# Performance work log

Measured on AMD Instinct MI355X. Metric: run time of the kernel, lower is better.

## Reference

```python
import jax, jax.numpy as jnp
import numpy as np

B, CIN, H, W = 32, 512, 16, 16
COUT, HEADS, SPARSITY = 2048, 8, 7
D = COUT // HEADS  # 256, must equal H*W
N = H * W


def conv1x1(x, w, b):
    # x: [B,C,H,W], w: [O,C], b: [O]
    return jnp.einsum('bchw,oc->bohw', x, w) + b[None, :, None, None]


def setup_inputs() -> dict:
    key = jax.random.key(0)
    ks = jax.random.split(key, 11)
    def lin(k, o, c):
        bound = 1.0 / np.sqrt(c)
        kw, kb = jax.random.split(k)
        return (jax.random.uniform(kw, (o, c), jnp.float32, -bound, bound),
                jax.random.uniform(kb, (o,), jnp.float32, -bound, bound))
    Wq, bq = lin(ks[0], COUT, CIN)
    Wk, bk = lin(ks[1], COUT, CIN)
    Wv, bv = lin(ks[2], COUT, CIN)
    Wo, bo = lin(ks[3], COUT, COUT)
    # kaiming_uniform_ on [COUT, COUT]
    gain = np.sqrt(2.0) / np.sqrt(5.0)  # default a=sqrt(5)
    bound = gain * np.sqrt(3.0 / COUT)
    coeff = jax.random.uniform(ks[4], (COUT, COUT), jnp.float32, -bound, bound)
    scale = jnp.array([np.sqrt(D)], jnp.float32)
    x = jax.random.normal(ks[5], (B, CIN, H, W), jnp.float32)
    return {"x": x, "Wq": Wq, "bq": bq, "Wk": Wk, "bk": bk, "Wv": Wv,
            "bv": bv, "Wo": Wo, "bo": bo, "coeff": coeff, "scale": scale}


def reference(x, Wq, bq, Wk, bk, Wv, bv, Wo, bo, coeff, scale):
    # enforce_sparsity: keep top-`SPARSITY` |coeff| per row, zero the rest
    _, idx = jax.lax.top_k(jnp.abs(coeff), SPARSITY)  # [COUT, SPARSITY]
    mask = jnp.zeros(coeff.shape, bool).at[jnp.arange(COUT)[:, None], idx].set(True)
    coeff_s = jnp.where(mask, coeff, 0.0)

    q = conv1x1(x, Wq, bq).reshape(B, HEADS, D, N)
    k = conv1x1(x, Wk, bk).reshape(B, HEADS, D, N)
    v = conv1x1(x, Wv, bv).reshape(B, HEADS, D, N)

    attn = jnp.einsum('bhdn,bhdm->bhnm', q, k) / scale[0]  # [B,h,N,N]
    sparse_attn = jnp.einsum('bhnm,mp->bhnp', attn, coeff_s[:D, :D])
    sparse_attn = jax.nn.softmax(sparse_attn, axis=-1)
    out = jnp.einsum('bhnm,bhmd->bhnd', sparse_attn, v.transpose(0, 1, 3, 2))
    out = out.transpose(0, 1, 3, 2).reshape(B, COUT, H, W)
    return conv1x1(out, Wo, bo)
```

## Files before the change

kernel.cpp:

```cpp
#include <hip/hip_runtime.h>

typedef unsigned short ushort;
typedef __attribute__((ext_vector_type(8))) short short8;
typedef __attribute__((ext_vector_type(8))) unsigned short ushort8;
typedef __attribute__((ext_vector_type(4))) unsigned short ushort4v;
typedef __attribute__((ext_vector_type(4))) float fx4;

#define MAXNNZ (256*7)

__device__ __forceinline__ ushort f2bf(float f) {
    union { float f; unsigned u; } v; v.f = f;
    unsigned r = v.u + 0x7fffu + ((v.u >> 16) & 1u);
    return (ushort)(r >> 16);
}

__device__ __forceinline__ float bf2f(ushort b) {
    union { unsigned u; float f; } v; v.u = ((unsigned)b) << 16;
    return v.f;
}

__device__ __forceinline__ void gload_lds16(const ushort* g, ushort* l) {
    __builtin_amdgcn_global_load_lds(
        (const __attribute__((address_space(1))) unsigned int*)g,
        (__attribute__((address_space(3))) unsigned int*)l, 16, 0, 0);
}

__global__ __launch_bounds__(256)
void topk_kernel(const float* __restrict__ coeff,
                 int* __restrict__ coo_cnt, int* __restrict__ coo_m,
                 int* __restrict__ coo_p, float* __restrict__ coo_v)
{
    int row = blockIdx.x;
    int tid = threadIdx.x;
    const float* crow = coeff + (long)row * 2048;
    float av[8];
#pragma unroll
    for (int i = 0; i < 8; ++i) av[i] = fabsf(crow[tid + 256 * i]);
    __shared__ unsigned long long red[256];
    for (int t = 0; t < 7; ++t) {
        float mx = -1.f; int mi = 0;
#pragma unroll
        for (int i = 0; i < 8; ++i) if (av[i] > mx) { mx = av[i]; mi = i; }
        unsigned col = (unsigned)(tid + 256 * mi);
        unsigned long long pk = ((unsigned long long)__float_as_uint(mx) << 32)
                              | (unsigned long long)(2048u - col);
        red[tid] = pk; __syncthreads();
        for (int s = 128; s > 0; s >>= 1) {
            if (tid < s) { if (red[tid + s] > red[tid]) red[tid] = red[tid + s]; }
            __syncthreads();
        }
        unsigned long long w = red[0];
        __syncthreads();
        unsigned wcol = 2048u - (unsigned)(w & 0xffffffffu);
        if ((wcol & 255u) == (unsigned)tid) av[wcol >> 8] = -1.f;
        if (tid == 0 && wcol < 256u) {
            int pos = atomicAdd(coo_cnt, 1);
            coo_m[pos] = row; coo_p[pos] = (int)wcol; coo_v[pos] = crow[wcol];
        }
    }
}

__global__ __launch_bounds__(256)
void csc_kernel(const int* __restrict__ coo_cnt, const int* __restrict__ coo_m,
                const int* __restrict__ coo_p, const float* __restrict__ coo_v,
                int* __restrict__ csc_ptr, int* __restrict__ csc_m, float* __restrict__ csc_v)
{
    __shared__ int cnt[256];
    __shared__ int off[257];
    __shared__ int cur[256];
    int tid = threadIdx.x;
    cnt[tid] = 0;
    __syncthreads();
    int n = *coo_cnt; if (n > MAXNNZ) n = MAXNNZ;
    for (int e = tid; e < n; e += 256) atomicAdd(&cnt[coo_p[e]], 1);
    __syncthreads();
    if (tid == 0) {
        int s = 0;
        for (int p = 0; p < 256; ++p) { off[p] = s; s += cnt[p]; }
        off[256] = s;
    }
    __syncthreads();
    csc_ptr[tid] = off[tid];
    if (tid == 0) csc_ptr[256] = off[256];
    cur[tid] = off[tid];
    __syncthreads();
    for (int e = tid; e < n; e += 256) {
        int p = coo_p[e];
        int pos = atomicAdd(&cur[p], 1);
        csc_m[pos] = coo_m[e];
        csc_v[pos] = coo_v[e];
    }
}

__global__ void cvt4_kernel(const float* a0, ushort* d0, int n0,
                            const float* a1, ushort* d1, int n1,
                            const float* a2, ushort* d2, int n2,
                            const float* a3, ushort* d3, int n3)
{
    const float* s; ushort* d; int n;
    switch (blockIdx.y) {
        case 0: s = a0; d = d0; n = n0; break;
        case 1: s = a1; d = d1; n = n1; break;
        case 2: s = a2; d = d2; n = n2; break;
        default: s = a3; d = d3; n = n3; break;
    }
    int nv = n >> 2;
    for (int i = blockIdx.x * blockDim.x + threadIdx.x; i < nv; i += gridDim.x * blockDim.x) {
        fx4 v = ((const fx4*)s)[i];
        ushort4v o;
        o[0] = f2bf(v[0]); o[1] = f2bf(v[1]); o[2] = f2bf(v[2]); o[3] = f2bf(v[3]);
        ((ushort4v*)d)[i] = o;
    }
}

__global__ __launch_bounds__(256)
void transpose_f32_bf16(const float* __restrict__ in, ushort* __restrict__ out, int R, int C)
{
    int z = blockIdx.z;
    const float* ib = in + (long)z * R * C;
    ushort* ob = out + (long)z * R * C;
    __shared__ ushort tile[64][72];
    int r0 = blockIdx.x * 64, c0 = blockIdx.y * 64;
    int tid = threadIdx.x;
    int rl = tid >> 2, sg = tid & 3;
#pragma unroll
    for (int h = 0; h < 4; ++h) {
        fx4 v = *(const fx4*)(ib + (long)(r0 + rl) * C + c0 + h * 16 + sg * 4);
#pragma unroll
        for (int i = 0; i < 4; ++i) tile[h * 16 + sg * 4 + i][rl] = f2bf(v[i]);
    }
    __syncthreads();
    int cl = rl;
#pragma unroll
    for (int h = 0; h < 2; ++h) {
        ushort8 vv = *(const ushort8*)(&tile[cl][h * 32 + sg * 8]);
        *(ushort8*)(ob + (long)(c0 + cl) * R + r0 + h * 32 + sg * 8) = vv;
    }
}

__global__ __launch_bounds__(256)
void kcomb_kernel(const ushort* __restrict__ kbT, ushort* __restrict__ ktc,
                  const int* __restrict__ csc_ptr, const int* __restrict__ csc_m,
                  const float* __restrict__ csc_v)
{
    int z = blockIdx.y;
    int tid = threadIdx.x;
    int p = blockIdx.x * 64 + (tid >> 2);
    int d0 = (tid & 3) * 64;
    const ushort* src = kbT + (long)z * 65536;
    float acc[64];
#pragma unroll
    for (int i = 0; i < 64; ++i) acc[i] = 0.f;
    int e0 = csc_ptr[p], e1 = csc_ptr[p + 1];
    for (int e = e0; e < e1; ++e) {
        const ushort* row = src + csc_m[e] * 256 + d0;
        float c = csc_v[e];
#pragma unroll
        for (int u = 0; u < 8; ++u) {
            ushort8 v = *(const ushort8*)(row + u * 8);
#pragma unroll
            for (int t = 0; t < 8; ++t) acc[u * 8 + t] += bf2f(v[t]) * c;
        }
    }
    ushort* dst = ktc + (long)z * 65536 + (long)p * 256 + d0;
#pragma unroll
    for (int u = 0; u < 8; ++u) {
        ushort8 o;
#pragma unroll
        for (int t = 0; t < 8; ++t) o[t] = f2bf(acc[u * 8 + t]);
        *(ushort8*)(dst + u * 8) = o;
    }
}

template<int MODE>
__global__ __launch_bounds__(256)
void gemm128(const ushort* __restrict__ A, long long strideA,
             const ushort* __restrict__ B, long long strideB,
             void* __restrict__ C,
             const float* __restrict__ bias0, const float* __restrict__ bias1,
             const float* __restrict__ bias2,
             int N, int K)
{
    int z = blockIdx.z;
    const ushort* Ab = A + (long long)z * strideA;
    const ushort* Bb = B + (long long)z * strideB;
    int m0 = blockIdx.x * 128, n0 = blockIdx.y * 128;

    __shared__ __align__(16) ushort As[128 * 32];
    __shared__ __align__(16) ushort Bs[128 * 32];
    __shared__ __align__(16) ushort Ct[(MODE == 3) ? 128 * 136 : 8];

    int tid = threadIdx.x;
    int wave = tid >> 6, lane = tid & 63;
    int wrow = wave >> 1, wcol = wave & 1;
    int l16 = lane & 15, quad = lane >> 4;
    int lrow = lane >> 2, lkq = lane & 3;

    fx4 acc[4][4];
#pragma unroll
    for (int i = 0; i < 4; ++i)
#pragma unroll
        for (int j = 0; j < 4; ++j) acc[i][j] = (fx4){0.f, 0.f, 0.f, 0.f};

    const ushort* gA0 = Ab + (long)(m0 + wave * 16 + lrow) * K + lkq * 8;
    const ushort* gA1 = gA0 + (long)64 * K;
    const ushort* gB0 = Bb + (long)(n0 + wave * 16 + lrow) * K + lkq * 8;
    const ushort* gB1 = gB0 + (long)64 * K;
    ushort* lA0 = As + (wave * 16) * 32;
    ushort* lA1 = As + (64 + wave * 16) * 32;
    ushort* lB0 = Bs + (wave * 16) * 32;
    ushort* lB1 = Bs + (64 + wave * 16) * 32;

    for (int kc = 0; kc < K; kc += 32) {
        __syncthreads();
        gload_lds16(gA0 + kc, lA0);
        gload_lds16(gA1 + kc, lA1);
        gload_lds16(gB0 + kc, lB0);
        gload_lds16(gB1 + kc, lB1);
        __syncthreads();

        short8 af[4], bf[4];
#pragma unroll
        for (int i = 0; i < 4; ++i)
            af[i] = *(const short8*)(As + (wrow * 64 + i * 16 + l16) * 32 + quad * 8);
#pragma unroll
        for (int j = 0; j < 4; ++j)
            bf[j] = *(const short8*)(Bs + (wcol * 64 + j * 16 + l16) * 32 + quad * 8);
#pragma unroll
        for (int i = 0; i < 4; ++i)
#pragma unroll
            for (int j = 0; j < 4; ++j)
                acc[i][j] = __builtin_amdgcn_mfma_f32_16x16x32_bf16(af[i], bf[j], acc[i][j], 0, 0, 0);
    }

    if (MODE == 3) {
#pragma unroll
        for (int i = 0; i < 4; ++i)
#pragma unroll
            for (int j = 0; j < 4; ++j) {
                int ml = wrow * 64 + i * 16 + quad * 4;
                int nl = wcol * 64 + j * 16 + l16;
                ushort4v pk;
#pragma unroll
                for (int r = 0; r < 4; ++r) pk[r] = f2bf(acc[i][j][r]);
                *(ushort4v*)(Ct + nl * 136 + ml) = pk;
            }
        __syncthreads();
        long long zb = z >> 3; int zh = z & 7;
        int nl = tid >> 3, mc = (tid & 7) * 16;
#pragma unroll
        for (int p4 = 0; p4 < 4; ++p4) {
            int n = p4 * 32 + nl;
            ushort8 v0 = *(const ushort8*)(Ct + n * 136 + mc);
            ushort8 v1 = *(const ushort8*)(Ct + n * 136 + mc + 8);
            ushort* dst = (ushort*)C + zb * 524288 + (long)(n0 + n) * 2048
                        + zh * 256 + m0 + mc;
            *(ushort8*)dst = v0;
            *(ushort8*)(dst + 8) = v1;
        }
        return;
    }
}

template<int MODE>
__global__ __launch_bounds__(512, 2)
void gemm256(const ushort* __restrict__ A, const ushort* __restrict__ B,
             void* __restrict__ C,
             const float* __restrict__ bias0, const float* __restrict__ bias1,
             const float* __restrict__ bias2,
             int MT, int K)
{
    __shared__ __align__(16) ushort lds[4][2][8192];

    int nwg = gridDim.x;
    int bid = blockIdx.x;
    int cpx = nwg >> 3;
    int swz = (bid & 7) * cpx + (bid >> 3);
    int mt = swz % MT, nt = swz / MT;
    int m0 = mt << 8, n0 = nt << 8;

    int tid = threadIdx.x;
    int wave = tid >> 6, lane = tid & 63;
    int wr = wave >> 2, wc = wave & 3;
    int l16 = lane & 15, quad = lane >> 4;

    int lc = (((lane & 3) ^ ((lane >> 3) & 3))) * 8;
    const ushort* gA0 = A + (long long)(m0 + wave * 16 + (lane >> 2)) * K + lc;
    const ushort* gA1 = gA0 + (long long)128 * K;
    const ushort* gB0 = B + (long long)(n0 + wave * 16 + (lane >> 2)) * K + lc;
    const ushort* gB1 = gB0 + (long long)128 * K;
    int ldso = wave * 512;

    int rsw = ((l16 >> 1) & 3) * 8;
    int aoff = (wr * 128 + l16) * 32 + ((quad * 8) ^ rsw);
    int boff = (wc * 64 + l16) * 32 + ((quad * 8) ^ rsw);

    fx4 acc[8][4];
#pragma unroll
    for (int i = 0; i < 8; ++i)
#pragma unroll
        for (int j = 0; j < 4; ++j) acc[i][j] = (fx4){0.f, 0.f, 0.f, 0.f};

    auto stageA = [&](int b, int kc) {
        gload_lds16(gA0 + kc, &lds[b][0][ldso]);
        gload_lds16(gA1 + kc, &lds[b][0][4096 + ldso]);
    };
    auto stageB = [&](int b, int kc) {
        gload_lds16(gB0 + kc, &lds[b][1][ldso]);
        gload_lds16(gB1 + kc, &lds[b][1][4096 + ldso]);
    };

    short8 af[4], bf[4];
    auto readA = [&](int b, int half) {
        const ushort* p = &lds[b][0][aoff + half * 2048];
#pragma unroll
        for (int i = 0; i < 4; ++i) af[i] = *(const short8*)(p + i * 512);
    };
    auto readB = [&](int b) {
        const ushort* p = &lds[b][1][boff];
#pragma unroll
        for (int j = 0; j < 4; ++j) bf[j] = *(const short8*)(p + j * 512);
    };
    auto mma = [&](int half) {
        __builtin_amdgcn_s_setprio(1);
#pragma unroll
        for (int i = 0; i < 4; ++i)
#pragma unroll
            for (int j = 0; j < 4; ++j)
                acc[half * 4 + i][j] =
                    __builtin_amdgcn_mfma_f32_16x16x32_bf16(af[i], bf[j], acc[half * 4 + i][j], 0, 0, 0);
        __builtin_amdgcn_s_setprio(0);
    };

    int NT = K >> 5;
    stageA(0, 0);  stageB(0, 0);
    stageA(1, 32); stageB(1, 32);
    stageA(2, 64); stageB(2, 64);
    asm volatile("s_waitcnt vmcnt(8)" ::: "memory");
    __builtin_amdgcn_s_barrier();

    for (int t = 0; t < NT; ++t) {
        int b = t & 3;
        readA(b, 0); readB(b);
        if (t + 3 < NT) stageA((t + 3) & 3, (t + 3) << 5);
        __builtin_amdgcn_s_barrier();
        asm volatile("s_waitcnt lgkmcnt(0)" ::: "memory");
        __builtin_amdgcn_sched_barrier(0);
        mma(0);
        __builtin_amdgcn_s_barrier();
        readA(b, 1);
        if (t + 3 < NT) {
            stageB((t + 3) & 3, (t + 3) << 5);
            asm volatile("s_waitcnt vmcnt(8)" ::: "memory");
        } else if (t + 2 < NT) {
            asm volatile("s_waitcnt vmcnt(4)" ::: "memory");
        } else if (t + 1 < NT) {
            asm volatile("s_waitcnt vmcnt(0)" ::: "memory");
        }
        __builtin_amdgcn_s_barrier();
        asm volatile("s_waitcnt lgkmcnt(0)" ::: "memory");
        __builtin_amdgcn_sched_barrier(0);
        mma(1);
        __builtin_amdgcn_s_barrier();
    }

    if (MODE == 5) {
        float* Cf = (float*)C + (long long)nt * 524288;
#pragma unroll
        for (int i = 0; i < 8; ++i) {
            int m = m0 + wr * 128 + i * 16 + quad * 4;
#pragma unroll
            for (int j = 0; j < 4; ++j) {
                int n = wc * 64 + j * 16 + l16;
                float* dst = Cf + (long long)m * 256 + n;
#pragma unroll
                for (int r = 0; r < 4; ++r)
                    dst[(long)r * 256] = acc[i][j][r] + bias0[m + r];
            }
        }
        return;
    }

    if (MODE == 4) {
        int sec = m0 >> 11;
        int ms0 = m0 & 2047;
        ushort* ct = &lds[0][0][0];
        if (sec < 2) {
            const float* bs = (sec == 0) ? bias0 : bias1;
            ushort* base = (ushort*)C + (long long)sec * 16777216
                         + (long long)nt * 524288 + (long long)(ms0 >> 8) * 65536;
#pragma unroll
            for (int hh = 0; hh < 2; ++hh) {
                if ((wc >> 1) == hh) {
#pragma unroll
                    for (int i = 0; i < 8; ++i)
#pragma unroll
                        for (int j = 0; j < 4; ++j) {
                            int nl = (wc & 1) * 64 + j * 16 + l16;
                            int ml = wr * 128 + i * 16 + quad * 4;
                            ushort4v pk;
#pragma unroll
                            for (int r = 0; r < 4; ++r)
                                pk[r] = f2bf(acc[i][j][r] + bs[ms0 + ml + r]);
                            *(ushort4v*)(ct + nl * 264 + ml) = pk;
                        }
                }
                __syncthreads();
                int row = tid & 127, c0 = (tid >> 7) * 64;
                ushort* dst = base + (long long)(hh * 128 + row) * 256 + c0;
                const ushort* src = ct + row * 264 + c0;
#pragma unroll
                for (int u = 0; u < 8; ++u)
                    *(ushort8*)(dst + u * 8) = *(const ushort8*)(src + u * 8);
                __syncthreads();
            }
        } else {
            ushort* base = (ushort*)C + 33554432LL + (long long)nt * 524288
                         + (long long)ms0 * 256;
#pragma unroll
            for (int hh = 0; hh < 2; ++hh) {
                if (wr == hh) {
#pragma unroll
                    for (int i = 0; i < 8; ++i)
#pragma unroll
                        for (int j = 0; j < 4; ++j) {
                            int nl = wc * 64 + j * 16 + l16;
                            int ml = i * 16 + quad * 4;
#pragma unroll
                            for (int r = 0; r < 4; ++r)
                                ct[(ml + r) * 264 + nl] =
                                    f2bf(acc[i][j][r] + bias2[ms0 + hh * 128 + ml + r]);
                        }
                }
                __syncthreads();
                int row = tid & 127, c0 = (tid >> 7) * 64;
                ushort* dst = base + (long long)(hh * 128 + row) * 256 + c0;
                const ushort* src = ct + row * 264 + c0;
#pragma unroll
                for (int u = 0; u < 8; ++u)
                    *(ushort8*)(dst + u * 8) = *(const ushort8*)(src + u * 8);
                __syncthreads();
            }
        }
        return;
    }
}

__global__ __launch_bounds__(256)
void tsm_kernel(const ushort* __restrict__ Q, const ushort* __restrict__ Kt,
                ushort* __restrict__ P, const float* __restrict__ scale_src)
{
    int z = blockIdx.y;
    const ushort* Ab = Q + (long)z * 65536;
    const ushort* Bb = Kt + (long)z * 65536;
    int n0 = blockIdx.x * 128;

    __shared__ __align__(16) ushort As[128 * 32];
    __shared__ __align__(16) ushort Bs[256 * 32];
    __shared__ float rmax[2][128];
    __shared__ float rsum[2][128];

    int tid = threadIdx.x;
    int wave = tid >> 6, lane = tid & 63;
    int wrow = wave >> 1, wcol = wave & 1;
    int l16 = lane & 15, quad = lane >> 4;
    int lrow = lane >> 2, lkq = lane & 3;

    fx4 acc[4][8];
#pragma unroll
    for (int i = 0; i < 4; ++i)
#pragma unroll
        for (int j = 0; j < 8; ++j) acc[i][j] = (fx4){0.f, 0.f, 0.f, 0.f};

    const ushort* gA0 = Ab + (long)(n0 + wave * 16 + lrow) * 256 + lkq * 8;
    const ushort* gA1 = gA0 + 64 * 256;
    const ushort* gB0 = Bb + (long)(wave * 16 + lrow) * 256 + lkq * 8;
    ushort* lA0 = As + (wave * 16) * 32;
    ushort* lA1 = As + (64 + wave * 16) * 32;
    ushort* lB0 = Bs + (wave * 16) * 32;

    for (int kc = 0; kc < 256; kc += 32) {
        __syncthreads();
        gload_lds16(gA0 + kc, lA0);
        gload_lds16(gA1 + kc, lA1);
        gload_lds16(gB0 + kc, lB0);
        gload_lds16(gB0 + 64 * 256 + kc, lB0 + 64 * 32);
        gload_lds16(gB0 + 128 * 256 + kc, lB0 + 128 * 32);
        gload_lds16(gB0 + 192 * 256 + kc, lB0 + 192 * 32);
        __syncthreads();

        short8 af[4], bf[8];
#pragma unroll
        for (int i = 0; i < 4; ++i)
            af[i] = *(const short8*)(As + (wrow * 64 + i * 16 + l16) * 32 + quad * 8);
#pragma unroll
        for (int j = 0; j < 8; ++j)
            bf[j] = *(const short8*)(Bs + (wcol * 128 + j * 16 + l16) * 32 + quad * 8);
#pragma unroll
        for (int i = 0; i < 4; ++i)
#pragma unroll
            for (int j = 0; j < 8; ++j)
                acc[i][j] = __builtin_amdgcn_mfma_f32_16x16x32_bf16(af[i], bf[j], acc[i][j], 0, 0, 0);
    }

    float sc = 1.0f / scale_src[0];
#pragma unroll
    for (int i = 0; i < 4; ++i)
#pragma unroll
        for (int j = 0; j < 8; ++j)
#pragma unroll
            for (int r = 0; r < 4; ++r) acc[i][j][r] *= sc;

    float lm[4][4];
#pragma unroll
    for (int i = 0; i < 4; ++i)
#pragma unroll
        for (int r = 0; r < 4; ++r) {
            float m = -1e30f;
#pragma unroll
            for (int j = 0; j < 8; ++j) m = fmaxf(m, acc[i][j][r]);
            lm[i][r] = m;
        }
#pragma unroll
    for (int d = 1; d < 16; d <<= 1)
#pragma unroll
        for (int i = 0; i < 4; ++i)
#pragma unroll
            for (int r = 0; r < 4; ++r) lm[i][r] = fmaxf(lm[i][r], __shfl_xor(lm[i][r], d, 16));
    if (l16 == 0) {
#pragma unroll
        for (int i = 0; i < 4; ++i)
#pragma unroll
            for (int r = 0; r < 4; ++r)
                rmax[wcol][wrow * 64 + i * 16 + quad * 4 + r] = lm[i][r];
    }
    __syncthreads();

    float ls[4][4];
#pragma unroll
    for (int i = 0; i < 4; ++i)
#pragma unroll
        for (int r = 0; r < 4; ++r) {
            int row = wrow * 64 + i * 16 + quad * 4 + r;
            float M = fmaxf(rmax[0][row], rmax[1][row]);
            float s = 0.f;
#pragma unroll
            for (int j = 0; j < 8; ++j) {
                float e = __expf(acc[i][j][r] - M);
                acc[i][j][r] = e;
                s += e;
            }
            ls[i][r] = s;
        }
#pragma unroll
    for (int d = 1; d < 16; d <<= 1)
#pragma unroll
        for (int i = 0; i < 4; ++i)
#pragma unroll
            for (int r = 0; r < 4; ++r) ls[i][r] += __shfl_xor(ls[i][r], d, 16);
    if (l16 == 0) {
#pragma unroll
        for (int i = 0; i < 4; ++i)
#pragma unroll
            for (int r = 0; r < 4; ++r)
                rsum[wcol][wrow * 64 + i * 16 + quad * 4 + r] = ls[i][r];
    }
    __syncthreads();

    ushort* Pb = P + (long)z * 65536;
#pragma unroll
    for (int i = 0; i < 4; ++i)
#pragma unroll
        for (int r = 0; r < 4; ++r) {
            int row = wrow * 64 + i * 16 + quad * 4 + r;
            float inv = 1.0f / (rsum[0][row] + rsum[1][row]);
#pragma unroll
            for (int j = 0; j < 8; ++j)
                Pb[(long)(n0 + row) * 256 + wcol * 128 + j * 16 + l16] = f2bf(acc[i][j][r] * inv);
        }
}

extern "C" void kernel_launch(void* const* d_in, const int* in_sizes, int n_in,
                              void* d_out, int out_size, void* d_ws, size_t ws_size,
                              hipStream_t stream)
{
    const float* x     = (const float*)d_in[0];
    const float* Wq    = (const float*)d_in[1];
    const float* bq    = (const float*)d_in[2];
    const float* Wk    = (const float*)d_in[3];
    const float* bk    = (const float*)d_in[4];
    const float* Wv    = (const float*)d_in[5];
    const float* bv    = (const float*)d_in[6];
    const float* Wo    = (const float*)d_in[7];
    const float* bo    = (const float*)d_in[8];
    const float* coeff = (const float*)d_in[9];
    const float* scale = (const float*)d_in[10];
    float* out = (float*)d_out;

    size_t o = 0;
    char* w = (char*)d_ws;
    auto take = [&](size_t bytes) -> void* {
        void* p = w + o; o += (bytes + 255) & ~(size_t)255; return p;
    };
    int*    coo_cnt = (int*)take(4);
    int*    coo_m   = (int*)take(MAXNNZ * 4);
    int*    coo_p   = (int*)take(MAXNNZ * 4);
    float*  coo_v   = (float*)take(MAXNNZ * 4);
    int*    csc_ptr = (int*)take(257 * 4);
    int*    csc_m   = (int*)take(MAXNNZ * 4);
    float*  csc_v   = (float*)take(MAXNNZ * 4);
    ushort* wqkv = (ushort*)take(6144L * 512 * 2);
    ushort* wob  = (ushort*)take(2048L * 2048 * 2);
    ushort* xT   = (ushort*)take(32L * 256 * 512 * 2);
    ushort* qkv  = (ushort*)take(3 * 16777216L * 2);
    ushort* qbT = qkv;
    ushort* kbT = qkv + 16777216L;
    ushort* vb  = qkv + 33554432L;
    ushort* ktc = (ushort*)take(16777216L * 2);
    ushort* P_ws = kbT;
    ushort* obT  = qbT;
    (void)in_sizes; (void)n_in; (void)out_size; (void)ws_size;

    hipMemsetAsync(coo_cnt, 0, 4, stream);
    topk_kernel<<<256, 256, 0, stream>>>(coeff, coo_cnt, coo_m, coo_p, coo_v);
    csc_kernel<<<1, 256, 0, stream>>>(coo_cnt, coo_m, coo_p, coo_v, csc_ptr, csc_m, csc_v);

    cvt4_kernel<<<dim3(1024, 4, 1), 256, 0, stream>>>(
        Wq, wqkv, 2048 * 512, Wk, wqkv + 2048L * 512, 2048 * 512,
        Wv, wqkv + 4096L * 512, 2048 * 512, Wo, wob, 2048 * 2048);
    transpose_f32_bf16<<<dim3(8, 4, 32), 256, 0, stream>>>(x, xT, 512, 256);

    gemm256<4><<<dim3(768, 1, 1), dim3(512, 1, 1), 0, stream>>>(
        wqkv, xT, qkv, bq, bk, bv, 24, 512);

    kcomb_kernel<<<dim3(4, 256), 256, 0, stream>>>(kbT, ktc, csc_ptr, csc_m, csc_v);

    tsm_kernel<<<dim3(2, 256), 256, 0, stream>>>(qbT, ktc, P_ws, scale);

    gemm128<3><<<dim3(2, 2, 256), 256, 0, stream>>>(
        vb, 65536, P_ws, 65536, obT, nullptr, nullptr, nullptr, 256, 256);

    gemm256<5><<<dim3(256, 1, 1), dim3(512, 1, 1), 0, stream>>>(
        wob, obT, out, bo, nullptr, nullptr, 8, 2048);
}
```

Before: 386.3 us.

## Fuse QK^T softmax and PV GEMM into one attention kernel keeping P in LDS

```diff
diff --git a/kernel.cpp b/kernel.cpp
--- a/kernel.cpp
+++ b/kernel.cpp
@@ -172,93 +172,207 @@
     }
 }
 
-template<int MODE>
-__global__ __launch_bounds__(256)
-void gemm128(const ushort* __restrict__ A, long long strideA,
-             const ushort* __restrict__ B, long long strideB,
-             void* __restrict__ C,
-             const float* __restrict__ bias0, const float* __restrict__ bias1,
-             const float* __restrict__ bias2,
-             int N, int K)
-{
-    int z = blockIdx.z;
-    const ushort* Ab = A + (long long)z * strideA;
-    const ushort* Bb = B + (long long)z * strideB;
-    int m0 = blockIdx.x * 128, n0 = blockIdx.y * 128;
-
+__global__ __launch_bounds__(512)
+void attn_kernel(const ushort* __restrict__ Q, const ushort* __restrict__ Kt,
+                 const ushort* __restrict__ V, ushort* __restrict__ O,
+                 const float* __restrict__ scale_src)
+{
+    int z = blockIdx.x;
+    int b = z >> 3, h = z & 7;
+    const ushort* Qz = Q + (long)z * 65536;
+    const ushort* Kz = Kt + (long)z * 65536;
+    const ushort* Vz = V + (long)b * 524288 + (long)h * 65536;
+    ushort* Ob = O + (long)b * 524288 + (long)h * 256;
+
+    __shared__ __align__(16) ushort P[128 * 256];
     __shared__ __align__(16) ushort As[128 * 32];
-    __shared__ __align__(16) ushort Bs[128 * 32];
-    __shared__ __align__(16) ushort Ct[(MODE == 3) ? 128 * 136 : 8];
+    __shared__ __align__(16) ushort Bs[256 * 32];
+    __shared__ __align__(16) ushort Vst[2][256 * 32];
+    __shared__ float rmax[4][128];
+    __shared__ float rsum[4][128];
 
     int tid = threadIdx.x;
     int wave = tid >> 6, lane = tid & 63;
-    int wrow = wave >> 1, wcol = wave & 1;
     int l16 = lane & 15, quad = lane >> 4;
-    int lrow = lane >> 2, lkq = lane & 3;
-
-    fx4 acc[4][4];
-#pragma unroll
-    for (int i = 0; i < 4; ++i)
-#pragma unroll
-        for (int j = 0; j < 4; ++j) acc[i][j] = (fx4){0.f, 0.f, 0.f, 0.f};
-
-    const ushort* gA0 = Ab + (long)(m0 + wave * 16 + lrow) * K + lkq * 8;
-    const ushort* gA1 = gA0 + (long)64 * K;
-    const ushort* gB0 = Bb + (long)(n0 + wave * 16 + lrow) * K + lkq * 8;
-    const ushort* gB1 = gB0 + (long)64 * K;
-    ushort* lA0 = As + (wave * 16) * 32;
-    ushort* lA1 = As + (64 + wave * 16) * 32;
-    ushort* lB0 = Bs + (wave * 16) * 32;
-    ushort* lB1 = Bs + (64 + wave * 16) * 32;
-
-    for (int kc = 0; kc < K; kc += 32) {
+
+    int skey = (tid >> 3) & 3;
+    int scol = ((tid & 3) ^ skey) * 8;
+    int srow = tid >> 2;
+    const ushort* qsrc  = Qz + (long)srow * 256 + scol;
+    const ushort* ksrc0 = Kz + (long)srow * 256 + scol;
+    const ushort* ksrc1 = ksrc0 + 128 * 256;
+    const ushort* vsrc0 = Vz + (long)srow * 256 + scol;
+    const ushort* vsrc1 = vsrc0 + 128 * 256;
+    ushort* aDst  = As + wave * 512;
+    ushort* bDst0 = Bs + wave * 512;
+    ushort* bDst1 = Bs + 4096 + wave * 512;
+
+    int rk = (l16 >> 1) & 3;
+    float sc = 1.0f / scale_src[0];
+
+    for (int hf = 0; hf < 2; ++hf) {
+        int wrow = wave >> 2, wcol = wave & 3;
+        fx4 acc[4][4];
+#pragma unroll
+        for (int i = 0; i < 4; ++i)
+#pragma unroll
+            for (int j = 0; j < 4; ++j) acc[i][j] = (fx4){0.f, 0.f, 0.f, 0.f};
+
+        const ushort* qs = qsrc + (long)hf * 128 * 256;
+        for (int kc = 0; kc < 256; kc += 32) {
+            __syncthreads();
+            gload_lds16(qs + kc, aDst);
+            gload_lds16(ksrc0 + kc, bDst0);
+            gload_lds16(ksrc1 + kc, bDst1);
+            __syncthreads();
+            short8 af[4], bf[4];
+#pragma unroll
+            for (int i = 0; i < 4; ++i)
+                af[i] = *(const short8*)(As + (wrow * 64 + i * 16 + l16) * 32 + ((quad ^ rk) * 8));
+#pragma unroll
+            for (int j = 0; j < 4; ++j)
+                bf[j] = *(const short8*)(Bs + (wcol * 64 + j * 16 + l16) * 32 + ((quad ^ rk) * 8));
+#pragma unroll
+            for (int i = 0; i < 4; ++i)
+#pragma unroll
+                for (int j = 0; j < 4; ++j)
+                    acc[i][j] = __builtin_amdgcn_mfma_f32_16x16x32_bf16(af[i], bf[j], acc[i][j], 0, 0, 0);
+        }
+
+#pragma unroll
+        for (int i = 0; i < 4; ++i)
+#pragma unroll
+            for (int j = 0; j < 4; ++j)
+#pragma unroll
+                for (int r = 0; r < 4; ++r) acc[i][j][r] *= sc;
+
+        float lm[4][4];
+#pragma unroll
+        for (int i = 0; i < 4; ++i)
+#pragma unroll
+            for (int r = 0; r < 4; ++r) {
+                float m = -1e30f;
+#pragma unroll
+                for (int j = 0; j < 4; ++j) m = fmaxf(m, acc[i][j][r]);
+                lm[i][r] = m;
+            }
+#pragma unroll
+        for (int d = 1; d < 16; d <<= 1)
+#pragma unroll
+            for (int i = 0; i < 4; ++i)
+#pragma unroll
+                for (int r = 0; r < 4; ++r) lm[i][r] = fmaxf(lm[i][r], __shfl_xor(lm[i][r], d, 16));
+        if (l16 == 0) {
+#pragma unroll
+            for (int i = 0; i < 4; ++i)
+#pragma unroll
+                for (int r = 0; r < 4; ++r)
+                    rmax[wcol][wrow * 64 + i * 16 + quad * 4 + r] = lm[i][r];
+        }
         __syncthreads();
-        gload_lds16(gA0 + kc, lA0);
-        gload_lds16(gA1 + kc, lA1);
-        gload_lds16(gB0 + kc, lB0);
-        gload_lds16(gB1 + kc, lB1);
+
+        float ls[4][4];
+#pragma unroll
+        for (int i = 0; i < 4; ++i)
+#pragma unroll
+            for (int r = 0; r < 4; ++r) {
+                int row = wrow * 64 + i * 16 + quad * 4 + r;
+                float M = fmaxf(fmaxf(rmax[0][row], rmax[1][row]),
+                                fmaxf(rmax[2][row], rmax[3][row]));
+                float s = 0.f;
+#pragma unroll
+                for (int j = 0; j < 4; ++j) {
+                    float e = __expf(acc[i][j][r] - M);
+                    acc[i][j][r] = e;
+                    s += e;
+                }
+                ls[i][r] = s;
+            }
+#pragma unroll
+        for (int d = 1; d < 16; d <<= 1)
+#pragma unroll
+            for (int i = 0; i < 4; ++i)
+#pragma unroll
+                for (int r = 0; r < 4; ++r) ls[i][r] += __shfl_xor(ls[i][r], d, 16);
+        if (l16 == 0) {
+#pragma unroll
+            for (int i = 0; i < 4; ++i)
+#pragma unroll
+                for (int r = 0; r < 4; ++r)
+                    rsum[wcol][wrow * 64 + i * 16 + quad * 4 + r] = ls[i][r];
+        }
         __syncthreads();
 
-        short8 af[4], bf[4];
-#pragma unroll
-        for (int i = 0; i < 4; ++i)
-            af[i] = *(const short8*)(As + (wrow * 64 + i * 16 + l16) * 32 + quad * 8);
-#pragma unroll
-        for (int j = 0; j < 4; ++j)
-            bf[j] = *(const short8*)(Bs + (wcol * 64 + j * 16 + l16) * 32 + quad * 8);
-#pragma unroll
-        for (int i = 0; i < 4; ++i)
+#pragma unroll
+        for (int i = 0; i < 4; ++i)
+#pragma unroll
+            for (int r = 0; r < 4; ++r) {
+                int row = wrow * 64 + i * 16 + quad * 4 + r;
+                float inv = 1.0f / (rsum[0][row] + rsum[1][row] + rsum[2][row] + rsum[3][row]);
+                int key = row & 7;
+#pragma unroll
+                for (int j = 0; j < 4; ++j) {
+                    int p = wcol * 64 + j * 16 + l16;
+                    int idx = row * 256 + ((((p >> 3) ^ key) << 3) | (p & 7));
+                    P[idx] = f2bf(acc[i][j][r] * inv);
+                }
+            }
+        __syncthreads();
+
+        int r2 = wave >> 2, c2 = wave & 3;
+        fx4 acc2[4][4];
+#pragma unroll
+        for (int i = 0; i < 4; ++i)
+#pragma unroll
+            for (int j = 0; j < 4; ++j) acc2[i][j] = (fx4){0.f, 0.f, 0.f, 0.f};
+
+        gload_lds16(vsrc0, Vst[0] + wave * 512);
+        gload_lds16(vsrc1, Vst[0] + 4096 + wave * 512);
+        __syncthreads();
+
+        for (int kk = 0; kk < 8; ++kk) {
+            short8 pa[4], vf[4];
+#pragma unroll
+            for (int i = 0; i < 4; ++i) {
+                int row = r2 * 64 + i * 16 + l16;
+                pa[i] = *(const short8*)(P + row * 256 + (((kk * 4 + quad) ^ (l16 & 7)) * 8));
+            }
 #pragma unroll
             for (int j = 0; j < 4; ++j)
-                acc[i][j] = __builtin_amdgcn_mfma_f32_16x16x32_bf16(af[i], bf[j], acc[i][j], 0, 0, 0);
-    }
-
-    if (MODE == 3) {
+                vf[j] = *(const short8*)(Vst[kk & 1] + (c2 * 64 + j * 16 + l16) * 32 + ((quad ^ rk) * 8));
+            if (kk < 7) {
+                gload_lds16(vsrc0 + (kk + 1) * 32, Vst[(kk + 1) & 1] + wave * 512);
+                gload_lds16(vsrc1 + (kk + 1) * 32, Vst[(kk + 1) & 1] + 4096 + wave * 512);
+            }
+#pragma unroll
+            for (int i = 0; i < 4; ++i)
+#pragma unroll
+                for (int j = 0; j < 4; ++j)
+                    acc2[i][j] = __builtin_amdgcn_mfma_f32_16x16x32_bf16(pa[i], vf[j], acc2[i][j], 0, 0, 0);
+            __syncthreads();
+        }
+
 #pragma unroll
         for (int i = 0; i < 4; ++i)
 #pragma unroll
             for (int j = 0; j < 4; ++j) {
-                int ml = wrow * 64 + i * 16 + quad * 4;
-                int nl = wcol * 64 + j * 16 + l16;
-                ushort4v pk;
-#pragma unroll
-                for (int r = 0; r < 4; ++r) pk[r] = f2bf(acc[i][j][r]);
-                *(ushort4v*)(Ct + nl * 136 + ml) = pk;
+                int rowb = r2 * 64 + i * 16 + quad * 4;
+                int col = c2 * 64 + j * 16 + l16;
+#pragma unroll
+                for (int rr = 0; rr < 4; ++rr) {
+                    int row = rowb + rr;
+                    int idx = row * 256 + ((((col >> 3) ^ (row & 7)) << 3) | (col & 7));
+                    P[idx] = f2bf(acc2[i][j][rr]);
+                }
             }
         __syncthreads();
-        long long zb = z >> 3; int zh = z & 7;
-        int nl = tid >> 3, mc = (tid & 7) * 16;
-#pragma unroll
-        for (int p4 = 0; p4 < 4; ++p4) {
-            int n = p4 * 32 + nl;
-            ushort8 v0 = *(const ushort8*)(Ct + n * 136 + mc);
-            ushort8 v1 = *(const ushort8*)(Ct + n * 136 + mc + 8);
-            ushort* dst = (ushort*)C + zb * 524288 + (long)(n0 + n) * 2048
-                        + zh * 256 + m0 + mc;
-            *(ushort8*)dst = v0;
-            *(ushort8*)(dst + 8) = v1;
-        }
-        return;
+#pragma unroll
+        for (int pass = 0; pass < 8; ++pass) {
+            int row = pass * 16 + (tid >> 5), ch = tid & 31;
+            ushort8 v = *(const ushort8*)(P + row * 256 + ((ch ^ (row & 7)) << 3));
+            *(ushort8*)(Ob + (long)(hf * 128 + row) * 2048 + ch * 8) = v;
+        }
+        __syncthreads();
     }
 }
 
@@ -444,140 +558,6 @@
         }
         return;
     }
-}
-
-__global__ __launch_bounds__(256)
-void tsm_kernel(const ushort* __restrict__ Q, const ushort* __restrict__ Kt,
-                ushort* __restrict__ P, const float* __restrict__ scale_src)
-{
-    int z = blockIdx.y;
-    const ushort* Ab = Q + (long)z * 65536;
-    const ushort* Bb = Kt + (long)z * 65536;
-    int n0 = blockIdx.x * 128;
-
-    __shared__ __align__(16) ushort As[128 * 32];
-    __shared__ __align__(16) ushort Bs[256 * 32];
-    __shared__ float rmax[2][128];
-    __shared__ float rsum[2][128];
-
-    int tid = threadIdx.x;
-    int wave = tid >> 6, lane = tid & 63;
-    int wrow = wave >> 1, wcol = wave & 1;
-    int l16 = lane & 15, quad = lane >> 4;
-    int lrow = lane >> 2, lkq = lane & 3;
-
-    fx4 acc[4][8];
-#pragma unroll
-    for (int i = 0; i < 4; ++i)
-#pragma unroll
-        for (int j = 0; j < 8; ++j) acc[i][j] = (fx4){0.f, 0.f, 0.f, 0.f};
-
-    const ushort* gA0 = Ab + (long)(n0 + wave * 16 + lrow) * 256 + lkq * 8;
-    const ushort* gA1 = gA0 + 64 * 256;
-    const ushort* gB0 = Bb + (long)(wave * 16 + lrow) * 256 + lkq * 8;
-    ushort* lA0 = As + (wave * 16) * 32;
-    ushort* lA1 = As + (64 + wave * 16) * 32;
-    ushort* lB0 = Bs + (wave * 16) * 32;
-
-    for (int kc = 0; kc < 256; kc += 32) {
-        __syncthreads();
-        gload_lds16(gA0 + kc, lA0);
-        gload_lds16(gA1 + kc, lA1);
-        gload_lds16(gB0 + kc, lB0);
-        gload_lds16(gB0 + 64 * 256 + kc, lB0 + 64 * 32);
-        gload_lds16(gB0 + 128 * 256 + kc, lB0 + 128 * 32);
-        gload_lds16(gB0 + 192 * 256 + kc, lB0 + 192 * 32);
-        __syncthreads();
-
-        short8 af[4], bf[8];
-#pragma unroll
-        for (int i = 0; i < 4; ++i)
-            af[i] = *(const short8*)(As + (wrow * 64 + i * 16 + l16) * 32 + quad * 8);
-#pragma unroll
-        for (int j = 0; j < 8; ++j)
-            bf[j] = *(const short8*)(Bs + (wcol * 128 + j * 16 + l16) * 32 + quad * 8);
-#pragma unroll
-        for (int i = 0; i < 4; ++i)
-#pragma unroll
-            for (int j = 0; j < 8; ++j)
-                acc[i][j] = __builtin_amdgcn_mfma_f32_16x16x32_bf16(af[i], bf[j], acc[i][j], 0, 0, 0);
-    }
-
-    float sc = 1.0f / scale_src[0];
-#pragma unroll
-    for (int i = 0; i < 4; ++i)
-#pragma unroll
-        for (int j = 0; j < 8; ++j)
-#pragma unroll
-            for (int r = 0; r < 4; ++r) acc[i][j][r] *= sc;
-
-    float lm[4][4];
-#pragma unroll
-    for (int i = 0; i < 4; ++i)
-#pragma unroll
-        for (int r = 0; r < 4; ++r) {
-            float m = -1e30f;
-#pragma unroll
-            for (int j = 0; j < 8; ++j) m = fmaxf(m, acc[i][j][r]);
-            lm[i][r] = m;
-        }
-#pragma unroll
-    for (int d = 1; d < 16; d <<= 1)
-#pragma unroll
-        for (int i = 0; i < 4; ++i)
-#pragma unroll
-            for (int r = 0; r < 4; ++r) lm[i][r] = fmaxf(lm[i][r], __shfl_xor(lm[i][r], d, 16));
-    if (l16 == 0) {
-#pragma unroll
-        for (int i = 0; i < 4; ++i)
-#pragma unroll
-            for (int r = 0; r < 4; ++r)
-                rmax[wcol][wrow * 64 + i * 16 + quad * 4 + r] = lm[i][r];
-    }
-    __syncthreads();
-
-    float ls[4][4];
-#pragma unroll
-    for (int i = 0; i < 4; ++i)
-#pragma unroll
-        for (int r = 0; r < 4; ++r) {
-            int row = wrow * 64 + i * 16 + quad * 4 + r;
-            float M = fmaxf(rmax[0][row], rmax[1][row]);
-            float s = 0.f;
-#pragma unroll
-            for (int j = 0; j < 8; ++j) {
-                float e = __expf(acc[i][j][r] - M);
-                acc[i][j][r] = e;
-                s += e;
-            }
-            ls[i][r] = s;
-        }
-#pragma unroll
-    for (int d = 1; d < 16; d <<= 1)
-#pragma unroll
-        for (int i = 0; i < 4; ++i)
-#pragma unroll
-            for (int r = 0; r < 4; ++r) ls[i][r] += __shfl_xor(ls[i][r], d, 16);
-    if (l16 == 0) {
-#pragma unroll
-        for (int i = 0; i < 4; ++i)
-#pragma unroll
-            for (int r = 0; r < 4; ++r)
-                rsum[wcol][wrow * 64 + i * 16 + quad * 4 + r] = ls[i][r];
-    }
-    __syncthreads();
-
-    ushort* Pb = P + (long)z * 65536;
-#pragma unroll
-    for (int i = 0; i < 4; ++i)
-#pragma unroll
-        for (int r = 0; r < 4; ++r) {
-            int row = wrow * 64 + i * 16 + quad * 4 + r;
-            float inv = 1.0f / (rsum[0][row] + rsum[1][row]);
-#pragma unroll
-            for (int j = 0; j < 8; ++j)
-                Pb[(long)(n0 + row) * 256 + wcol * 128 + j * 16 + l16] = f2bf(acc[i][j][r] * inv);
-        }
 }
 
 extern "C" void kernel_launch(void* const* d_in, const int* in_sizes, int n_in,
@@ -617,8 +597,7 @@
     ushort* kbT = qkv + 16777216L;
     ushort* vb  = qkv + 33554432L;
     ushort* ktc = (ushort*)take(16777216L * 2);
-    ushort* P_ws = kbT;
-    ushort* obT  = qbT;
+    ushort* obT  = kbT;
     (void)in_sizes; (void)n_in; (void)out_size; (void)ws_size;
 
     hipMemsetAsync(coo_cnt, 0, 4, stream);
@@ -635,10 +614,7 @@
 
     kcomb_kernel<<<dim3(4, 256), 256, 0, stream>>>(kbT, ktc, csc_ptr, csc_m, csc_v);
 
-    tsm_kernel<<<dim3(2, 256), 256, 0, stream>>>(qbT, ktc, P_ws, scale);
-
-    gemm128<3><<<dim3(2, 2, 256), 256, 0, stream>>>(
-        vb, 65536, P_ws, 65536, obT, nullptr, nullptr, nullptr, 256, 256);
+    attn_kernel<<<256, 512, 0, stream>>>(qbT, ktc, vb, obT, scale);
 
     gemm256<5><<<dim3(256, 1, 1), dim3(512, 1, 1), 0, stream>>>(
         wob, obT, out, bo, nullptr, nullptr, 8, 2048);
```

New measurement: 401.5 us. +3.9%, slower.
